# Optimization experiments

Hardware: AMD Instinct MI355X
Metric: run time of the kernel (lower is better)

## Reference

```python
import jax, jax.numpy as jnp
import numpy as np

B, IN_LEN, N_VARS, PRED_LEN, E, TOPK = 64, 1024, 512, 1024, 8, 2


def setup_inputs() -> dict:
    key = jax.random.key(0)
    k1, k2, k3, k4 = jax.random.split(key, 4)
    x = jax.random.normal(k1, (B, IN_LEN, N_VARS), dtype=jnp.float32)
    # Gating: nn.Linear(seq_len, n_experts, bias=False) -> store as [seq, E] (x @ gate_W)
    gate_W = jax.random.normal(k2, (IN_LEN, E), dtype=jnp.float32) / np.sqrt(IN_LEN).astype(np.float32)
    # experts: nn.Linear(seq_len, pred_len) each -> stacked [E, seq, pred], bias [E, pred]
    expert_W = jax.random.normal(k3, (E, IN_LEN, PRED_LEN), dtype=jnp.float32) / np.sqrt(IN_LEN).astype(np.float32)
    expert_b = jax.random.normal(k4, (E, PRED_LEN), dtype=jnp.float32) * 0.01
    return {"x": x, "gate_W": gate_W, "expert_W": expert_W, "expert_b": expert_b}


def reference(x, gate_W, expert_W, expert_b):
    # x: [B, in_len, n_vars] -> tokens are (batch, variable) pairs of length in_len
    xt = jnp.transpose(x, (0, 2, 1))                      # [B, N, S]
    gate = jax.nn.softmax(xt @ gate_W, axis=-1)           # [B, N, E] (softmaxed logits, as in torch code)
    weights, sel = jax.lax.top_k(gate, TOPK)              # [B, N, K]
    # combine[b,n,e] = sum_k weights[b,n,k] * 1[sel[b,n,k]==e]  (scatter of top-k weights)
    combine = jnp.sum(weights[..., None] * jax.nn.one_hot(sel, E, dtype=x.dtype), axis=2)  # [B, N, E]
    # masked dense combine: identical math to gather->Linear->weighted scatter-add
    out = jnp.zeros((xt.shape[0], xt.shape[1], PRED_LEN), dtype=x.dtype)
    for e in range(E):  # small fixed expert loop
        y_e = xt @ expert_W[e] + expert_b[e]              # [B, N, P]
        out = out + combine[:, :, e:e + 1] * y_e
    out = jnp.transpose(out, (0, 2, 1))                   # [B, pred_len, n_vars]
    gate_mean = jnp.mean(gate, axis=0)                    # [N, E] == gate_logits.mean(dim=0)
    return (out, gate_mean)
```

## Files before the change

kernel.cpp:

```cpp
#include <hip/hip_runtime.h>
#include <cstddef>

typedef __bf16 bf16x8 __attribute__((ext_vector_type(8)));
typedef float  f32x4  __attribute__((ext_vector_type(4)));
typedef unsigned short u16x8 __attribute__((ext_vector_type(8)));

#define GLOBAL_AS __attribute__((address_space(1)))
#define LDS_AS    __attribute__((address_space(3)))

__device__ __forceinline__ void gload_lds16(const void* g, void* l) {
    __builtin_amdgcn_global_load_lds((const GLOBAL_AS unsigned int*)g,
                                     (LDS_AS unsigned int*)l, 16, 0, 0);
}

__device__ __forceinline__ unsigned short f2bf(float f) {
    union { float f; unsigned int u; } v; v.f = f;
    unsigned int r = v.u + 0x7FFFu + ((v.u >> 16) & 1u);
    return (unsigned short)(r >> 16);
}
__device__ __forceinline__ float bf2f(unsigned short h) {
    union { unsigned int u; float f; } v; v.u = ((unsigned int)h) << 16;
    return v.f;
}

__global__ __launch_bounds__(256) void transpose_cast_kernel(
    const float* __restrict__ src, unsigned short* __restrict__ dst,
    int R, int C)
{
    const int bat = blockIdx.z;
    src += (size_t)bat * R * C;
    dst += (size_t)bat * R * C;
    const int r0 = blockIdx.y * 64, c0 = blockIdx.x * 64;
    __shared__ float t[64][65];
    const int tid = threadIdx.x;
    const int rr = tid >> 4;
    const int cc = (tid & 15) * 4;

    #pragma unroll
    for (int p = 0; p < 4; p++) {
        int r = p * 16 + rr;
        const float4 v = *reinterpret_cast<const float4*>(&src[(size_t)(r0 + r) * C + c0 + cc]);
        t[r][cc + 0] = v.x; t[r][cc + 1] = v.y; t[r][cc + 2] = v.z; t[r][cc + 3] = v.w;
    }
    __syncthreads();
    #pragma unroll
    for (int p = 0; p < 4; p++) {
        int c = p * 16 + rr;
        ushort4 o;
        o.x = f2bf(t[cc + 0][c]); o.y = f2bf(t[cc + 1][c]);
        o.z = f2bf(t[cc + 2][c]); o.w = f2bf(t[cc + 3][c]);
        *reinterpret_cast<ushort4*>(&dst[(size_t)(c0 + c) * R + r0 + cc]) = o;
    }
}

__global__ __launch_bounds__(256) void transpose_x_gate_kernel(
    const float* __restrict__ src, const float* __restrict__ gW,
    unsigned short* __restrict__ dst, float* __restrict__ plog)
{
    const int bat = blockIdx.z;
    const int R = 1024, C = 512;
    const float* srcb = src + (size_t)bat * R * C;
    unsigned short* dstb = dst + (size_t)bat * R * C;
    const int r0 = blockIdx.y * 64, c0 = blockIdx.x * 64;
    __shared__ float t[64][65];
    __shared__ float gWs[64][8];
    __shared__ float pacc[4][64][9];
    const int tid = threadIdx.x;
    const int rr = tid >> 4;
    const int cc = (tid & 15) * 4;

    if (tid < 128) {
        reinterpret_cast<float4*>(&gWs[0][0])[tid] =
            reinterpret_cast<const float4*>(gW + (size_t)r0 * 8)[tid];
    }
    #pragma unroll
    for (int p = 0; p < 4; p++) {
        int r = p * 16 + rr;
        const float4 v = *reinterpret_cast<const float4*>(&srcb[(size_t)(r0 + r) * C + c0 + cc]);
        t[r][cc + 0] = v.x; t[r][cc + 1] = v.y; t[r][cc + 2] = v.z; t[r][cc + 3] = v.w;
    }
    __syncthreads();
    #pragma unroll
    for (int p = 0; p < 4; p++) {
        int c = p * 16 + rr;
        ushort4 o;
        o.x = f2bf(t[cc + 0][c]); o.y = f2bf(t[cc + 1][c]);
        o.z = f2bf(t[cc + 2][c]); o.w = f2bf(t[cc + 3][c]);
        *reinterpret_cast<ushort4*>(&dstb[(size_t)(c0 + c) * R + r0 + cc]) = o;
    }

    {
        const int nl = tid & 63;
        const int sc = tid >> 6;
        float a[8];
        #pragma unroll
        for (int e = 0; e < 8; e++) a[e] = 0.f;
        for (int s = sc * 16; s < sc * 16 + 16; s++) {
            float xv = t[s][nl];
            #pragma unroll
            for (int e = 0; e < 8; e++) a[e] = fmaf(xv, gWs[s][e], a[e]);
        }
        #pragma unroll
        for (int e = 0; e < 8; e++) pacc[sc][nl][e] = a[e];
        __syncthreads();
        if (tid < 64) {
            const size_t base = (((size_t)bat * 16 + blockIdx.y) * 512 + c0 + tid) * 8;
            #pragma unroll
            for (int e = 0; e < 8; e++) {
                float v = ((pacc[0][tid][e] + pacc[1][tid][e]) + pacc[2][tid][e]) + pacc[3][tid][e];
                plog[base + e] = v;
            }
        }
    }
}

__global__ __launch_bounds__(256) void gate_stage2_kernel(
    const float* __restrict__ plog,
    float* __restrict__ gate, int* __restrict__ e01,
    float* __restrict__ w0a, float* __restrict__ w1a,
    int* __restrict__ hist)
{
    __shared__ int h[16];
    const int tid = threadIdx.x;
    if (tid < 16) h[tid] = 0;
    __syncthreads();

    const int t = blockIdx.x * 256 + tid;
    const int b = t >> 9;
    const int n = t & 511;

    float acc[8];
    #pragma unroll
    for (int e = 0; e < 8; e++) acc[e] = 0.f;
    for (int y = 0; y < 16; y++) {
        const float* pp = plog + (((size_t)b * 16 + y) * 512 + n) * 8;
        const float4 lo = *reinterpret_cast<const float4*>(pp);
        const float4 hi = *reinterpret_cast<const float4*>(pp + 4);
        acc[0] += lo.x; acc[1] += lo.y; acc[2] += lo.z; acc[3] += lo.w;
        acc[4] += hi.x; acc[5] += hi.y; acc[6] += hi.z; acc[7] += hi.w;
    }
    float m = acc[0];
    #pragma unroll
    for (int e = 1; e < 8; e++) m = fmaxf(m, acc[e]);
    float p[8], s = 0.f;
    #pragma unroll
    for (int e = 0; e < 8; e++) { p[e] = __expf(acc[e] - m); s += p[e]; }
    float inv = 1.f / s;
    #pragma unroll
    for (int e = 0; e < 8; e++) p[e] *= inv;

    int e0 = 0;
    #pragma unroll
    for (int e = 1; e < 8; e++) if (p[e] > p[e0]) e0 = e;
    int e1 = -1;
    #pragma unroll
    for (int e = 0; e < 8; e++) {
        if (e == e0) continue;
        if (e1 < 0 || p[e] > p[e1]) e1 = e;
    }

    const size_t base = (size_t)t * 8;
    #pragma unroll
    for (int e = 0; e < 8; e++) gate[base + e] = p[e];
    e01[t] = e0 | (e1 << 8);
    w0a[t] = p[e0];
    w1a[t] = p[e1];

    atomicAdd(&h[e0], 1);
    atomicAdd(&h[8 + e1], 1);
    __syncthreads();
    if (tid < 16) hist[blockIdx.x * 16 + tid] = h[tid];
}

__global__ __launch_bounds__(256) void gate_mean_kernel(
    const float* __restrict__ gate, float* __restrict__ out)
{
    const int idx = blockIdx.x * 256 + threadIdx.x;
    float s = 0.f;
    #pragma unroll 8
    for (int b = 0; b < 64; b++) s += gate[(size_t)b * 4096 + idx];
    out[idx] = s * (1.f / 64.f);
}

__global__ __launch_bounds__(256) void scan_kernel(
    const int* __restrict__ hist, int* __restrict__ chunk_off,
    int* __restrict__ meta)
{
    __shared__ int cnt_s[16];
    const int tid = threadIdx.x;
    if (tid < 16) {
        int run = 0;
        for (int c = 0; c < 128; c++) {
            chunk_off[c * 16 + tid] = run;
            run += hist[c * 16 + tid];
        }
        cnt_s[tid] = run;
        meta[16 + tid] = run;
    }
    __syncthreads();
    __shared__ int base_s[16];
    if (tid == 0) {
        int run = 0, trun = 0;
        meta[32] = 0;
        for (int g = 0; g < 16; g++) {
            base_s[g] = run;
            meta[g] = run;
            run += cnt_s[g];
            trun += (cnt_s[g] + 127) >> 7;
            meta[33 + g] = trun;
        }
    }
    __syncthreads();
    for (int i = tid; i < 2048; i += 256)
        chunk_off[i] += base_s[i & 15];
}

__global__ __launch_bounds__(256) void fill_kernel(
    const int* __restrict__ e01, const int* __restrict__ chunk_off,
    int* __restrict__ perm, int* __restrict__ posA, int* __restrict__ posB)
{
    __shared__ int se0[256], se1[256];
    const int tid = threadIdx.x;
    const int chunk = blockIdx.x;
    const int t = chunk * 256 + tid;
    const int ev = e01[t];
    const int e0 = ev & 255, e1 = ev >> 8;
    se0[tid] = e0; se1[tid] = e1;
    __syncthreads();
    int r0 = 0, r1 = 0;
    for (int j = 0; j < 256; j++) {
        if (j >= tid) break;
        if (se0[j] == e0) r0++;
        if (se1[j] == e1) r1++;
    }
    const int p0 = chunk_off[chunk * 16 + e0] + r0;
    const int p1 = chunk_off[chunk * 16 + 8 + e1] + r1;
    perm[p0] = t; perm[p1] = t;
    posA[t] = p0; posB[t] = p1;
}

__global__ __launch_bounds__(256, 2) void grouped_gemm_kernel(
    const unsigned short* __restrict__ Wt,
    const unsigned short* __restrict__ xt,
    const int* __restrict__ perm,
    const int* __restrict__ meta,
    const float* __restrict__ expert_b,
    unsigned short* __restrict__ tmp)
{
    const int d   = blockIdx.x;
    const int xcd = d & 7;
    const int jj  = d >> 3;
    const int tile = xcd * 66 + (jj >> 3);
    const int p0   = (jj & 7) * 128;

    int g = -1;
    #pragma unroll
    for (int gg = 0; gg < 16; gg++) {
        if (tile >= meta[32 + gg] && tile < meta[33 + gg]) g = gg;
    }
    if (g < 0) return;
    const int lt = tile - meta[32 + g];
    const int e = g & 7;
    const int cnt_local = meta[16 + g] - lt * 128;
    const int pbase = meta[g] + lt * 128;

    __shared__ unsigned short As[128 * 64];
    __shared__ unsigned short Bs[128 * 64];

    const int tid  = threadIdx.x;
    const int wave = tid >> 6, lane = tid & 63;
    const int wr = wave >> 1, wc = wave & 1;
    const int q = lane >> 4, r16 = lane & 15;

    const int srow   = tid >> 3;
    const int schunk = tid & 7;
    const int gcol   = (schunk ^ (srow & 7)) * 8;

    const unsigned short* Abase = Wt + (size_t)e * 1024 * 1024;

    int tok[4];
    #pragma unroll
    for (int c = 0; c < 4; c++) {
        int row = c * 32 + srow;
        int idx = row < cnt_local ? row : 0;
        tok[c] = perm[pbase + idx];
    }

    f32x4 acc[4][4];
    #pragma unroll
    for (int m = 0; m < 4; m++)
        #pragma unroll
        for (int nn = 0; nn < 4; nn++)
            acc[m][nn] = (f32x4){0.f, 0.f, 0.f, 0.f};

    const int rsw = r16 & 7;

    for (int kt = 0; kt < 16; kt++) {
        __syncthreads();
        #pragma unroll
        for (int c = 0; c < 4; c++) {
            int row = c * 32 + srow;
            gload_lds16(Abase + (size_t)(p0 + row) * 1024 + kt * 64 + gcol,
                        &As[row * 64 + schunk * 8]);
        }
        #pragma unroll
        for (int c = 0; c < 4; c++) {
            int row = c * 32 + srow;
            gload_lds16(xt + (size_t)tok[c] * 1024 + kt * 64 + gcol,
                        &Bs[row * 64 + schunk * 8]);
        }
        __syncthreads();

        #pragma unroll
        for (int kk = 0; kk < 2; kk++) {
            const int ch = ((kk * 4 + q) ^ rsw) * 8;
            bf16x8 af[4], bfr[4];
            #pragma unroll
            for (int m = 0; m < 4; m++) {
                af[m]  = *reinterpret_cast<const bf16x8*>(&As[(wr * 64 + m * 16 + r16) * 64 + ch]);
                bfr[m] = *reinterpret_cast<const bf16x8*>(&Bs[(wc * 64 + m * 16 + r16) * 64 + ch]);
            }
            #pragma unroll
            for (int m = 0; m < 4; m++)
                #pragma unroll
                for (int nn = 0; nn < 4; nn++)
                    acc[m][nn] = __builtin_amdgcn_mfma_f32_16x16x32_bf16(
                        af[m], bfr[nn], acc[m][nn], 0, 0, 0);
        }
    }

    float bv[4][4];
    #pragma unroll
    for (int m = 0; m < 4; m++)
        #pragma unroll
        for (int r = 0; r < 4; r++)
            bv[m][r] = expert_b[e * 1024 + p0 + wr * 64 + m * 16 + q * 4 + r];

    #pragma unroll
    for (int nn = 0; nn < 4; nn++) {
        const int j = wc * 64 + nn * 16 + r16;
        if (j < cnt_local) {
            const size_t rowb = (size_t)(pbase + j) * 1024;
            #pragma unroll
            for (int m = 0; m < 4; m++) {
                ushort4 o;
                o.x = f2bf(acc[m][nn][0] + bv[m][0]);
                o.y = f2bf(acc[m][nn][1] + bv[m][1]);
                o.z = f2bf(acc[m][nn][2] + bv[m][2]);
                o.w = f2bf(acc[m][nn][3] + bv[m][3]);
                *reinterpret_cast<ushort4*>(&tmp[rowb + p0 + wr * 64 + m * 16 + q * 4]) = o;
            }
        }
    }
}

__global__ __launch_bounds__(256) void combine_kernel(
    const unsigned short* __restrict__ tmp,
    const int* __restrict__ posA, const int* __restrict__ posB,
    const float* __restrict__ w0a, const float* __restrict__ w1a,
    float* __restrict__ out)
{
    __shared__ unsigned short l0[64 * 128];
    __shared__ unsigned short l1[64 * 128];
    __shared__ float sw0[64], sw1[64];
    const int tid = threadIdx.x;
    const int b = blockIdx.z;
    const int p0 = blockIdx.y * 128;
    const int n0 = blockIdx.x * 64;

    if (tid < 64) {
        int t = b * 512 + n0 + tid;
        sw0[tid] = w0a[t];
        sw1[tid] = w1a[t];
    }

    #pragma unroll
    for (int pass = 0; pass < 8; pass++) {
        int rowid = pass * 16 + (tid >> 4);
        int slot = rowid >> 6, j = rowid & 63;
        int t = b * 512 + n0 + j;
        int pos = slot ? posB[t] : posA[t];
        u16x8 v = *reinterpret_cast<const u16x8*>(&tmp[(size_t)pos * 1024 + p0 + (tid & 15) * 8]);
        unsigned short* dst = slot ? l1 : l0;
        int c0 = (tid & 15) * 8;
        int sw = (j & 31) << 2;
        ushort4 a; a.x = v[0]; a.y = v[1]; a.z = v[2]; a.w = v[3];
        ushort4 bq; bq.x = v[4]; bq.y = v[5]; bq.z = v[6]; bq.w = v[7];
        *reinterpret_cast<ushort4*>(&dst[j * 128 + (c0 ^ sw)]) = a;
        *reinterpret_cast<ushort4*>(&dst[j * 128 + ((c0 + 4) ^ sw)]) = bq;
    }
    __syncthreads();

    const int j = tid & 63;
    const int wv = tid >> 6;
    const float wa = sw0[j], wb = sw1[j];
    const int sw = (j & 31) << 2;
    #pragma unroll 8
    for (int pp = 0; pp < 32; pp++) {
        int p = wv * 32 + pp;
        float v0 = bf2f(l0[j * 128 + (p ^ sw)]);
        float v1 = bf2f(l1[j * 128 + (p ^ sw)]);
        out[((size_t)b * 1024 + p0 + p) * 512 + n0 + j] = wa * v0 + wb * v1;
    }
}

__global__ __launch_bounds__(256, 2) void moe_dense_idx_kernel(
    const unsigned short* __restrict__ Wt,
    const unsigned short* __restrict__ xt,
    const int* __restrict__ e01,
    const float* __restrict__ w0a, const float* __restrict__ w1a,
    const float* __restrict__ expert_b,
    float* __restrict__ out)
{
    __shared__ unsigned short As[128 * 64];
    __shared__ unsigned short Bs[128 * 64];

    const int tid  = threadIdx.x;
    const int wave = tid >> 6, lane = tid & 63;
    const int wr = wave >> 1, wc = wave & 1;
    const int q = lane >> 4, r16 = lane & 15;
    const int b  = blockIdx.z;
    const int p0 = blockIdx.y * 128;
    const int n0 = blockIdx.x * 128;

    const unsigned short* Bbase = xt + (size_t)b * 512 * 1024;
    const int srow = tid >> 3;
    const int scol = (tid & 7) * 8;

    f32x4 out_acc[4][4];
    #pragma unroll
    for (int m = 0; m < 4; m++)
        #pragma unroll
        for (int nn = 0; nn < 4; nn++)
            out_acc[m][nn] = (f32x4){0.f, 0.f, 0.f, 0.f};

    for (int e = 0; e < 8; e++) {
        const unsigned short* Abase = Wt + (size_t)e * 1024 * 1024;
        f32x4 acc[4][4];
        #pragma unroll
        for (int m = 0; m < 4; m++)
            #pragma unroll
            for (int nn = 0; nn < 4; nn++)
                acc[m][nn] = (f32x4){0.f, 0.f, 0.f, 0.f};

        for (int kt = 0; kt < 16; kt++) {
            __syncthreads();
            #pragma unroll
            for (int c = 0; c < 4; c++) {
                int row = c * 32 + srow;
                gload_lds16(Abase + (size_t)(p0 + row) * 1024 + kt * 64 + scol,
                            &As[row * 64 + scol]);
            }
            #pragma unroll
            for (int c = 0; c < 4; c++) {
                int row = c * 32 + srow;
                gload_lds16(Bbase + (size_t)(n0 + row) * 1024 + kt * 64 + scol,
                            &Bs[row * 64 + scol]);
            }
            __syncthreads();
            #pragma unroll
            for (int kk = 0; kk < 2; kk++) {
                bf16x8 af[4], bfr[4];
                #pragma unroll
                for (int m = 0; m < 4; m++) {
                    af[m]  = *reinterpret_cast<const bf16x8*>(&As[(wr * 64 + m * 16 + r16) * 64 + kk * 32 + q * 8]);
                    bfr[m] = *reinterpret_cast<const bf16x8*>(&Bs[(wc * 64 + m * 16 + r16) * 64 + kk * 32 + q * 8]);
                }
                #pragma unroll
                for (int m = 0; m < 4; m++)
                    #pragma unroll
                    for (int nn = 0; nn < 4; nn++)
                        acc[m][nn] = __builtin_amdgcn_mfma_f32_16x16x32_bf16(
                            af[m], bfr[nn], acc[m][nn], 0, 0, 0);
            }
        }
        float cw[4], bv[4][4];
        #pragma unroll
        for (int nn = 0; nn < 4; nn++) {
            int t = b * 512 + n0 + wc * 64 + nn * 16 + r16;
            int ev = e01[t];
            cw[nn] = (e == (ev & 255)) ? w0a[t] : ((e == (ev >> 8)) ? w1a[t] : 0.f);
        }
        #pragma unroll
        for (int m = 0; m < 4; m++)
            #pragma unroll
            for (int r = 0; r < 4; r++)
                bv[m][r] = expert_b[e * 1024 + p0 + wr * 64 + m * 16 + q * 4 + r];
        #pragma unroll
        for (int m = 0; m < 4; m++)
            #pragma unroll
            for (int nn = 0; nn < 4; nn++)
                #pragma unroll
                for (int r = 0; r < 4; r++)
                    out_acc[m][nn][r] += cw[nn] * (acc[m][nn][r] + bv[m][r]);
    }
    #pragma unroll
    for (int m = 0; m < 4; m++)
        #pragma unroll
        for (int nn = 0; nn < 4; nn++)
            #pragma unroll
            for (int r = 0; r < 4; r++) {
                int p = p0 + wr * 64 + m * 16 + q * 4 + r;
                int n = n0 + wc * 64 + nn * 16 + r16;
                out[(size_t)b * 1024 * 512 + (size_t)p * 512 + n] = out_acc[m][nn][r];
            }
}

extern "C" void kernel_launch(void* const* d_in, const int* in_sizes, int n_in,
                              void* d_out, int out_size, void* d_ws, size_t ws_size,
                              hipStream_t stream) {
    const float* x        = (const float*)d_in[0];
    const float* gate_W   = (const float*)d_in[1];
    const float* expert_W = (const float*)d_in[2];
    const float* expert_b = (const float*)d_in[3];
    float* out = (float*)d_out;

    char* ws = (char*)d_ws;
    unsigned short* Wt  = (unsigned short*)(ws + 0);
    unsigned short* xt  = (unsigned short*)(ws + 16777216);
    float* gate  = (float*)(ws + 83886080);
    float* w0a   = (float*)(ws + 84934656);
    float* w1a   = (float*)(ws + 85065728);
    int*   e01   = (int*)(ws + 85196800);
    int*   hist  = (int*)(ws + 85327872);
    int*   coff  = (int*)(ws + 85336064);
    int*   meta  = (int*)(ws + 85344256);
    int*   perm  = (int*)(ws + 85344512);
    int*   posA  = (int*)(ws + 85606656);
    int*   posB  = (int*)(ws + 85737728);
    unsigned short* tmp = (unsigned short*)(ws + 85868800);
    float* plog = (float*)(ws + 85868800);
    const size_t NEEDED = 85868800ull + 134217728ull;

    transpose_cast_kernel<<<dim3(16, 16, 8), 256, 0, stream>>>(expert_W, Wt, 1024, 1024);
    transpose_x_gate_kernel<<<dim3(8, 16, 64), 256, 0, stream>>>(x, gate_W, xt, plog);

    gate_stage2_kernel<<<128, 256, 0, stream>>>(plog, gate, e01, w0a, w1a, hist);
    gate_mean_kernel<<<16, 256, 0, stream>>>(gate, out + 33554432);

    if (ws_size >= NEEDED) {
        scan_kernel<<<1, 256, 0, stream>>>(hist, coff, meta);
        fill_kernel<<<128, 256, 0, stream>>>(e01, coff, perm, posA, posB);
        grouped_gemm_kernel<<<dim3(4224), 256, 0, stream>>>(Wt, xt, perm, meta, expert_b, tmp);
        combine_kernel<<<dim3(8, 8, 64), 256, 0, stream>>>(tmp, posA, posB, w0a, w1a, out);
    } else {
        moe_dense_idx_kernel<<<dim3(4, 8, 64), 256, 0, stream>>>(Wt, xt, e01, w0a, w1a, expert_b, out);
    }
}
```

Before: 277.4 us.

## Enlarge grouped GEMM tiles to 256x256 with double-buffered LDS, ballot-based fill ranks

The grouped expert GEMM moves from 128x128 tiles with 256 threads to 256x256 tiles with 512 threads. It double-buffers the A/B staging in LDS, prefetching two k-steps ahead with explicit vmcnt waits, so global loads overlap MFMA work and each loaded tile is reused more. The scan's tile count and the grid size are adjusted to match. The fill kernel's quadratic rank loop is replaced by wave ballots plus per-wave histograms. In exchange, LDS use rises to 128KB per block and register pressure from 32 accumulators grows, and larger tiles waste more padding on partially filled expert groups.

```diff
diff --git a/kernel.cpp b/kernel.cpp
--- a/kernel.cpp
+++ b/kernel.cpp
@@ -206,7 +206,7 @@
             base_s[g] = run;
             meta[g] = run;
             run += cnt_s[g];
-            trun += (cnt_s[g] + 127) >> 7;
+            trun += (cnt_s[g] + 255) >> 8;
             meta[33 + g] = trun;
         }
     }
@@ -219,27 +219,42 @@
     const int* __restrict__ e01, const int* __restrict__ chunk_off,
     int* __restrict__ perm, int* __restrict__ posA, int* __restrict__ posB)
 {
-    __shared__ int se0[256], se1[256];
+    __shared__ int wh[4][16];
     const int tid = threadIdx.x;
+    const int wv = tid >> 6, lane = tid & 63;
     const int chunk = blockIdx.x;
     const int t = chunk * 256 + tid;
     const int ev = e01[t];
     const int e0 = ev & 255, e1 = ev >> 8;
-    se0[tid] = e0; se1[tid] = e1;
-    __syncthreads();
-    int r0 = 0, r1 = 0;
-    for (int j = 0; j < 256; j++) {
-        if (j >= tid) break;
-        if (se0[j] == e0) r0++;
-        if (se1[j] == e1) r1++;
-    }
-    const int p0 = chunk_off[chunk * 16 + e0] + r0;
-    const int p1 = chunk_off[chunk * 16 + 8 + e1] + r1;
+
+    const unsigned long long ltmask = (lane == 63) ? 0x7FFFFFFFFFFFFFFFull
+                                                   : ((1ull << lane) - 1ull);
+    unsigned long long m0sel = 0, m1sel = 0;
+    #pragma unroll
+    for (int e = 0; e < 8; e++) {
+        unsigned long long b0 = __ballot(e0 == e);
+        unsigned long long b1 = __ballot(e1 == e);
+        if (e0 == e) m0sel = b0;
+        if (e1 == e) m1sel = b1;
+        if (lane == 0) {
+            wh[wv][e]     = __popcll(b0);
+            wh[wv][8 + e] = __popcll(b1);
+        }
+    }
+    const int r0l = __popcll(m0sel & ltmask);
+    const int r1l = __popcll(m1sel & ltmask);
+    __syncthreads();
+
+    int off0 = 0, off1 = 0;
+    for (int w = 0; w < wv; w++) { off0 += wh[w][e0]; off1 += wh[w][8 + e1]; }
+
+    const int p0 = chunk_off[chunk * 16 + e0] + off0 + r0l;
+    const int p1 = chunk_off[chunk * 16 + 8 + e1] + off1 + r1l;
     perm[p0] = t; perm[p1] = t;
     posA[t] = p0; posB[t] = p1;
 }
 
-__global__ __launch_bounds__(256, 2) void grouped_gemm_kernel(
+__global__ __launch_bounds__(512, 2) void grouped_gemm_kernel(
     const unsigned short* __restrict__ Wt,
     const unsigned short* __restrict__ xt,
     const int* __restrict__ perm,
@@ -247,11 +262,11 @@
     const float* __restrict__ expert_b,
     unsigned short* __restrict__ tmp)
 {
-    const int d   = blockIdx.x;
-    const int xcd = d & 7;
-    const int jj  = d >> 3;
-    const int tile = xcd * 66 + (jj >> 3);
-    const int p0   = (jj & 7) * 128;
+    const int d    = blockIdx.x;
+    const int xcd  = d & 7;
+    const int jj   = d >> 3;
+    const int tile = xcd * 34 + (jj >> 2);
+    const int p0   = (jj & 3) * 256;
 
     int g = -1;
     #pragma unroll
@@ -261,15 +276,15 @@
     if (g < 0) return;
     const int lt = tile - meta[32 + g];
     const int e = g & 7;
-    const int cnt_local = meta[16 + g] - lt * 128;
-    const int pbase = meta[g] + lt * 128;
-
-    __shared__ unsigned short As[128 * 64];
-    __shared__ unsigned short Bs[128 * 64];
+    const int cnt_local = meta[16 + g] - lt * 256;
+    const int pbase = meta[g] + lt * 256;
+
+    __shared__ unsigned short As[2][256 * 64];
+    __shared__ unsigned short Bs[2][256 * 64];
 
     const int tid  = threadIdx.x;
-    const int wave = tid >> 6, lane = tid & 63;
-    const int wr = wave >> 1, wc = wave & 1;
+    const int wid  = tid >> 6, lane = tid & 63;
+    const int wr = wid >> 2, wc = wid & 3;
     const int q = lane >> 4, r16 = lane & 15;
 
     const int srow   = tid >> 3;
@@ -281,60 +296,82 @@
     int tok[4];
     #pragma unroll
     for (int c = 0; c < 4; c++) {
-        int row = c * 32 + srow;
+        int row = c * 64 + srow;
         int idx = row < cnt_local ? row : 0;
         tok[c] = perm[pbase + idx];
     }
 
-    f32x4 acc[4][4];
-    #pragma unroll
-    for (int m = 0; m < 4; m++)
+    f32x4 acc[8][4];
+    #pragma unroll
+    for (int m = 0; m < 8; m++)
         #pragma unroll
         for (int nn = 0; nn < 4; nn++)
             acc[m][nn] = (f32x4){0.f, 0.f, 0.f, 0.f};
 
+    #define STAGE(buf, kt) do {                                                   \
+        _Pragma("unroll")                                                         \
+        for (int c = 0; c < 4; c++) {                                             \
+            int row = c * 64 + srow;                                              \
+            gload_lds16(Abase + (size_t)(p0 + row) * 1024 + (kt) * 64 + gcol,     \
+                        &As[buf][row * 64 + schunk * 8]);                         \
+        }                                                                         \
+        _Pragma("unroll")                                                         \
+        for (int c = 0; c < 4; c++) {                                             \
+            int row = c * 64 + srow;                                              \
+            gload_lds16(xt + (size_t)tok[c] * 1024 + (kt) * 64 + gcol,            \
+                        &Bs[buf][row * 64 + schunk * 8]);                         \
+        }                                                                         \
+    } while (0)
+
     const int rsw = r16 & 7;
 
+    STAGE(0, 0);
+    STAGE(1, 1);
+    asm volatile("s_waitcnt vmcnt(8)" ::: "memory");
+    __builtin_amdgcn_sched_barrier(0);
+    __builtin_amdgcn_s_barrier();
+
+    #pragma unroll 2
     for (int kt = 0; kt < 16; kt++) {
-        __syncthreads();
-        #pragma unroll
-        for (int c = 0; c < 4; c++) {
-            int row = c * 32 + srow;
-            gload_lds16(Abase + (size_t)(p0 + row) * 1024 + kt * 64 + gcol,
-                        &As[row * 64 + schunk * 8]);
-        }
-        #pragma unroll
-        for (int c = 0; c < 4; c++) {
-            int row = c * 32 + srow;
-            gload_lds16(xt + (size_t)tok[c] * 1024 + kt * 64 + gcol,
-                        &Bs[row * 64 + schunk * 8]);
-        }
-        __syncthreads();
-
+        const int cur = kt & 1;
         #pragma unroll
         for (int kk = 0; kk < 2; kk++) {
             const int ch = ((kk * 4 + q) ^ rsw) * 8;
-            bf16x8 af[4], bfr[4];
-            #pragma unroll
-            for (int m = 0; m < 4; m++) {
-                af[m]  = *reinterpret_cast<const bf16x8*>(&As[(wr * 64 + m * 16 + r16) * 64 + ch]);
-                bfr[m] = *reinterpret_cast<const bf16x8*>(&Bs[(wc * 64 + m * 16 + r16) * 64 + ch]);
-            }
-            #pragma unroll
-            for (int m = 0; m < 4; m++)
+            bf16x8 af[8], bfr[4];
+            #pragma unroll
+            for (int m = 0; m < 8; m++)
+                af[m] = *reinterpret_cast<const bf16x8*>(
+                    &As[cur][(wr * 128 + m * 16 + r16) * 64 + ch]);
+            #pragma unroll
+            for (int nn = 0; nn < 4; nn++)
+                bfr[nn] = *reinterpret_cast<const bf16x8*>(
+                    &Bs[cur][(wc * 64 + nn * 16 + r16) * 64 + ch]);
+            #pragma unroll
+            for (int m = 0; m < 8; m++)
                 #pragma unroll
                 for (int nn = 0; nn < 4; nn++)
                     acc[m][nn] = __builtin_amdgcn_mfma_f32_16x16x32_bf16(
                         af[m], bfr[nn], acc[m][nn], 0, 0, 0);
         }
-    }
-
-    float bv[4][4];
-    #pragma unroll
-    for (int m = 0; m < 4; m++)
+        __builtin_amdgcn_sched_barrier(0);
+        __builtin_amdgcn_s_barrier();
+        if (kt < 14) {
+            STAGE(cur, kt + 2);
+            asm volatile("s_waitcnt vmcnt(8)" ::: "memory");
+        } else {
+            asm volatile("s_waitcnt vmcnt(0)" ::: "memory");
+        }
+        __builtin_amdgcn_sched_barrier(0);
+        __builtin_amdgcn_s_barrier();
+    }
+    #undef STAGE
+
+    float bv[8][4];
+    #pragma unroll
+    for (int m = 0; m < 8; m++)
         #pragma unroll
         for (int r = 0; r < 4; r++)
-            bv[m][r] = expert_b[e * 1024 + p0 + wr * 64 + m * 16 + q * 4 + r];
+            bv[m][r] = expert_b[e * 1024 + p0 + wr * 128 + m * 16 + q * 4 + r];
 
     #pragma unroll
     for (int nn = 0; nn < 4; nn++) {
@@ -342,13 +379,13 @@
         if (j < cnt_local) {
             const size_t rowb = (size_t)(pbase + j) * 1024;
             #pragma unroll
-            for (int m = 0; m < 4; m++) {
+            for (int m = 0; m < 8; m++) {
                 ushort4 o;
                 o.x = f2bf(acc[m][nn][0] + bv[m][0]);
                 o.y = f2bf(acc[m][nn][1] + bv[m][1]);
                 o.z = f2bf(acc[m][nn][2] + bv[m][2]);
                 o.w = f2bf(acc[m][nn][3] + bv[m][3]);
-                *reinterpret_cast<ushort4*>(&tmp[rowb + p0 + wr * 64 + m * 16 + q * 4]) = o;
+                *reinterpret_cast<ushort4*>(&tmp[rowb + p0 + wr * 128 + m * 16 + q * 4]) = o;
             }
         }
     }
@@ -541,7 +578,7 @@
     if (ws_size >= NEEDED) {
         scan_kernel<<<1, 256, 0, stream>>>(hist, coff, meta);
         fill_kernel<<<128, 256, 0, stream>>>(e01, coff, perm, posA, posB);
-        grouped_gemm_kernel<<<dim3(4224), 256, 0, stream>>>(Wt, xt, perm, meta, expert_b, tmp);
+        grouped_gemm_kernel<<<dim3(1088), 512, 0, stream>>>(Wt, xt, perm, meta, expert_b, tmp);
         combine_kernel<<<dim3(8, 8, 64), 256, 0, stream>>>(tmp, posA, posB, w0a, w1a, out);
     } else {
         moe_dense_idx_kernel<<<dim3(4, 8, 64), 256, 0, stream>>>(Wt, xt, e01, w0a, w1a, expert_b, out);
```

Result: slower. 315.6 us (+13.8%).

## Double-buffer gathered token tile in grouped GEMM and use ballot ranking in fill

Applied to the files above, without the earlier changes.

The grouped GEMM now keeps two LDS buffers for the gathered token (B) tile. The next k-step's B tile is issued with global_load_lds while the current step's MFMAs run, and manual waitcnt and barrier calls replace __syncthreads. The expert-weight (A) tile is still single-buffered and is loaded each iteration. Separately, fill_kernel replaces an O(256) per-thread serial rank loop with wave ballots plus a per-wave histogram prefix. The cost is more LDS for B and hand-written vmcnt counting that relies on the exact order loads are issued.

```diff
diff --git a/kernel.cpp b/kernel.cpp
--- a/kernel.cpp
+++ b/kernel.cpp
@@ -219,22 +219,37 @@
     const int* __restrict__ e01, const int* __restrict__ chunk_off,
     int* __restrict__ perm, int* __restrict__ posA, int* __restrict__ posB)
 {
-    __shared__ int se0[256], se1[256];
+    __shared__ int wh[4][16];
     const int tid = threadIdx.x;
+    const int wv = tid >> 6, lane = tid & 63;
     const int chunk = blockIdx.x;
     const int t = chunk * 256 + tid;
     const int ev = e01[t];
     const int e0 = ev & 255, e1 = ev >> 8;
-    se0[tid] = e0; se1[tid] = e1;
-    __syncthreads();
-    int r0 = 0, r1 = 0;
-    for (int j = 0; j < 256; j++) {
-        if (j >= tid) break;
-        if (se0[j] == e0) r0++;
-        if (se1[j] == e1) r1++;
-    }
-    const int p0 = chunk_off[chunk * 16 + e0] + r0;
-    const int p1 = chunk_off[chunk * 16 + 8 + e1] + r1;
+
+    const unsigned long long ltmask = (lane == 63) ? 0x7FFFFFFFFFFFFFFFull
+                                                   : ((1ull << lane) - 1ull);
+    unsigned long long m0sel = 0, m1sel = 0;
+    #pragma unroll
+    for (int e = 0; e < 8; e++) {
+        unsigned long long b0 = __ballot(e0 == e);
+        unsigned long long b1 = __ballot(e1 == e);
+        if (e0 == e) m0sel = b0;
+        if (e1 == e) m1sel = b1;
+        if (lane == 0) {
+            wh[wv][e]     = __popcll(b0);
+            wh[wv][8 + e] = __popcll(b1);
+        }
+    }
+    const int r0l = __popcll(m0sel & ltmask);
+    const int r1l = __popcll(m1sel & ltmask);
+    __syncthreads();
+
+    int off0 = 0, off1 = 0;
+    for (int w = 0; w < wv; w++) { off0 += wh[w][e0]; off1 += wh[w][8 + e1]; }
+
+    const int p0 = chunk_off[chunk * 16 + e0] + off0 + r0l;
+    const int p1 = chunk_off[chunk * 16 + 8 + e1] + off1 + r1l;
     perm[p0] = t; perm[p1] = t;
     posA[t] = p0; posB[t] = p1;
 }
@@ -265,12 +280,13 @@
     const int pbase = meta[g] + lt * 128;
 
     __shared__ unsigned short As[128 * 64];
-    __shared__ unsigned short Bs[128 * 64];
+    __shared__ unsigned short Bs[2][128 * 64];
 
     const int tid  = threadIdx.x;
     const int wave = tid >> 6, lane = tid & 63;
     const int wr = wave >> 1, wc = wave & 1;
     const int q = lane >> 4, r16 = lane & 15;
+    const int rsw = r16 & 7;
 
     const int srow   = tid >> 3;
     const int schunk = tid & 7;
@@ -293,23 +309,40 @@
         for (int nn = 0; nn < 4; nn++)
             acc[m][nn] = (f32x4){0.f, 0.f, 0.f, 0.f};
 
-    const int rsw = r16 & 7;
+    #define STAGE_A(kt) do {                                                      \
+        _Pragma("unroll")                                                         \
+        for (int c = 0; c < 4; c++) {                                             \
+            int row = c * 32 + srow;                                              \
+            gload_lds16(Abase + (size_t)(p0 + row) * 1024 + (kt) * 64 + gcol,     \
+                        &As[row * 64 + schunk * 8]);                              \
+        } } while (0)
+    #define STAGE_B(buf, kt) do {                                                 \
+        _Pragma("unroll")                                                         \
+        for (int c = 0; c < 4; c++) {                                             \
+            int row = c * 32 + srow;                                              \
+            gload_lds16(xt + (size_t)tok[c] * 1024 + (kt) * 64 + gcol,            \
+                        &Bs[buf][row * 64 + schunk * 8]);                         \
+        } } while (0)
+
+    STAGE_B(0, 0);
 
     for (int kt = 0; kt < 16; kt++) {
-        __syncthreads();
-        #pragma unroll
-        for (int c = 0; c < 4; c++) {
-            int row = c * 32 + srow;
-            gload_lds16(Abase + (size_t)(p0 + row) * 1024 + kt * 64 + gcol,
-                        &As[row * 64 + schunk * 8]);
-        }
-        #pragma unroll
-        for (int c = 0; c < 4; c++) {
-            int row = c * 32 + srow;
-            gload_lds16(xt + (size_t)tok[c] * 1024 + kt * 64 + gcol,
-                        &Bs[row * 64 + schunk * 8]);
-        }
-        __syncthreads();
+        const int cur = kt & 1;
+        asm volatile("s_waitcnt lgkmcnt(0)" ::: "memory");
+        __builtin_amdgcn_sched_barrier(0);
+        __builtin_amdgcn_s_barrier();
+        __builtin_amdgcn_sched_barrier(0);
+
+        STAGE_A(kt);
+        if (kt < 15) STAGE_B(cur ^ 1, kt + 1);
+        if (kt < 15) {
+            asm volatile("s_waitcnt vmcnt(4)" ::: "memory");
+        } else {
+            asm volatile("s_waitcnt vmcnt(0)" ::: "memory");
+        }
+        __builtin_amdgcn_sched_barrier(0);
+        __builtin_amdgcn_s_barrier();
+        __builtin_amdgcn_sched_barrier(0);
 
         #pragma unroll
         for (int kk = 0; kk < 2; kk++) {
@@ -318,7 +351,7 @@
             #pragma unroll
             for (int m = 0; m < 4; m++) {
                 af[m]  = *reinterpret_cast<const bf16x8*>(&As[(wr * 64 + m * 16 + r16) * 64 + ch]);
-                bfr[m] = *reinterpret_cast<const bf16x8*>(&Bs[(wc * 64 + m * 16 + r16) * 64 + ch]);
+                bfr[m] = *reinterpret_cast<const bf16x8*>(&Bs[cur][(wc * 64 + m * 16 + r16) * 64 + ch]);
             }
             #pragma unroll
             for (int m = 0; m < 4; m++)
@@ -328,6 +361,8 @@
                         af[m], bfr[nn], acc[m][nn], 0, 0, 0);
         }
     }
+    #undef STAGE_A
+    #undef STAGE_B
 
     float bv[4][4];
     #pragma unroll
```

Result: slower. 289.0 us (+4.2%).
